# Kernel optimization log

Measured on AMD Instinct MI355X. Metric: run time of the kernel, lower is better.

Reference implementation:

```python
import jax, jax.numpy as jnp
import numpy as np

EPS = 1e-5


def _conv1x1(x, w, b):
    # x: (B,C,H,W), w: (O,C), b: (O,)
    return jnp.einsum('bchw,oc->bohw', x, w) + b[None, :, None, None]


def setup_inputs() -> dict:
    key = jax.random.key(0)
    ks = jax.random.split(key, 12)
    C, Ci = 512, 256
    B, H, W = 4, 64, 64
    s_in = 1.0 / np.sqrt(C)
    s_ci = 1.0 / np.sqrt(Ci)
    return {
        'x': jax.random.normal(ks[0], (B, C, H, W), dtype=jnp.float32),
        'g_w': jax.random.normal(ks[1], (Ci, C), dtype=jnp.float32) * s_in,
        'g_b': jax.random.normal(ks[2], (Ci,), dtype=jnp.float32) * 0.01,
        'theta_w': jax.random.normal(ks[3], (Ci, C), dtype=jnp.float32) * s_in,
        'theta_b': jax.random.normal(ks[4], (Ci,), dtype=jnp.float32) * 0.01,
        'phi_w': jax.random.normal(ks[5], (Ci, C), dtype=jnp.float32) * s_in,
        'phi_b': jax.random.normal(ks[6], (Ci,), dtype=jnp.float32) * 0.01,
        'W_w': jax.random.normal(ks[7], (C, Ci), dtype=jnp.float32) * s_ci,
        'W_b': jax.random.normal(ks[8], (C,), dtype=jnp.float32) * 0.01,
        'bn_gamma': jax.random.normal(ks[9], (C,), dtype=jnp.float32) * 0.1,
        'bn_beta': jax.random.normal(ks[10], (C,), dtype=jnp.float32) * 0.01,
    }


def reference(x, g_w, g_b, theta_w, theta_b, phi_w, phi_b, W_w, W_b, bn_gamma, bn_beta):
    B, C, H, W = x.shape
    Ci = g_w.shape[0]
    HW = H * W
    # 1x1-conv projections -> token form
    g = _conv1x1(x, g_w, g_b).reshape(B, Ci, HW).transpose(0, 2, 1)        # (B,HW,Ci)
    theta = _conv1x1(x, theta_w, theta_b).reshape(B, Ci, HW).transpose(0, 2, 1)  # (B,HW,Ci)
    phi = _conv1x1(x, phi_w, phi_b).reshape(B, Ci, HW)                      # (B,Ci,HW)
    # dense HWxHW attention, scaled by sqrt(inter_channels)
    pairwise = jnp.einsum('bnc,bcm->bnm', theta, phi) / jnp.sqrt(jnp.float32(Ci))
    attn = jax.nn.softmax(pairwise, axis=-1)
    y = jnp.einsum('bnm,bmc->bnc', attn, g)                                 # (B,HW,Ci)
    y = y.transpose(0, 2, 1).reshape(B, Ci, H, W)
    # output 1x1 conv + BatchNorm2d (training-mode batch statistics)
    z = _conv1x1(y, W_w, W_b)
    mean = jnp.mean(z, axis=(0, 2, 3), keepdims=True)
    var = jnp.var(z, axis=(0, 2, 3), keepdims=True)
    z = bn_gamma[None, :, None, None] * (z - mean) * jax.lax.rsqrt(var + EPS) + bn_beta[None, :, None, None]
    return z + x
```

## Files before the change

kernel.cpp:

```cpp
#include <hip/hip_runtime.h>

typedef unsigned short u16;
typedef __attribute__((ext_vector_type(4))) u16 u16x4;
typedef __attribute__((ext_vector_type(8))) u16 u16x8;
typedef __attribute__((ext_vector_type(8))) short s16x8;
typedef __attribute__((ext_vector_type(4))) float f32x4;

#define B_  4
#define C_  512
#define CI_ 256
#define HW_ 4096

static __device__ __forceinline__ u16 f2bf(float f) {
  unsigned u = __float_as_uint(f);
  return (u16)((u + 0x7FFFu + ((u >> 16) & 1u)) >> 16);
}
static __device__ __forceinline__ float bf2f(u16 h) {
  return __uint_as_float(((unsigned)h) << 16);
}

static __device__ __forceinline__ f32x4 mfma16(s16x8 a, s16x8 b, f32x4 c) {
  return __builtin_amdgcn_mfma_f32_16x16x32_bf16(a, b, c, 0, 0, 0);
}

typedef __attribute__((address_space(3))) unsigned int as3_u32;
typedef const __attribute__((address_space(1))) unsigned int as1_u32;
static __device__ __forceinline__ void gload16(const u16* g, u16* l) {
  __builtin_amdgcn_global_load_lds((as1_u32*)g, (as3_u32*)l, 16, 0, 0);
}

__global__ __launch_bounds__(256) void k0_wcvt(
    const float* __restrict__ wg, const float* __restrict__ wt,
    const float* __restrict__ wp, const float* __restrict__ Ww,
    u16* __restrict__ wB, u16* __restrict__ WwB)
{
  int idx = (blockIdx.x * 256 + threadIdx.x) * 8;
  const float* src;
  u16* dst;
  if (idx < 393216) {
    int r = idx >> 17;
    src = (r == 0 ? wg : r == 1 ? wt : wp) + (idx & 131071);
    dst = wB + idx;
  } else {
    src = Ww + (idx - 393216);
    dst = WwB + (idx - 393216);
  }
  float4 v0 = *reinterpret_cast<const float4*>(src);
  float4 v1 = *reinterpret_cast<const float4*>(src + 4);
  u16x8 h;
  h[0] = f2bf(v0.x); h[1] = f2bf(v0.y); h[2] = f2bf(v0.z); h[3] = f2bf(v0.w);
  h[4] = f2bf(v1.x); h[5] = f2bf(v1.y); h[6] = f2bf(v1.z); h[7] = f2bf(v1.w);
  *reinterpret_cast<u16x8*>(dst) = h;
}

__global__ __launch_bounds__(256) void k0_xt(
    const float* __restrict__ x, u16* __restrict__ xT, int b0)
{
  __shared__ u16 lds[64][72];
  const int tid = threadIdx.x;
  const int n0 = blockIdx.x * 64, c0 = blockIdx.y * 64;
  const int bl = blockIdx.z;
  const int b = b0 + bl;
  const int nc = (tid & 15) * 4;
#pragma unroll
  for (int i = 0; i < 4; ++i) {
    int cr = (tid >> 4) + i * 16;
    float4 v = *reinterpret_cast<const float4*>(
        &x[((size_t)(b * C_ + c0 + cr)) * HW_ + n0 + nc]);
    u16x4 h; h[0] = f2bf(v.x); h[1] = f2bf(v.y); h[2] = f2bf(v.z); h[3] = f2bf(v.w);
    *reinterpret_cast<u16x4*>(&lds[cr][nc]) = h;
  }
  __syncthreads();
  const int n = tid & 63, cg = tid >> 6;
  u16x8 o0, o1;
#pragma unroll
  for (int j = 0; j < 8; ++j) { o0[j] = lds[cg * 16 + j][n]; o1[j] = lds[cg * 16 + 8 + j][n]; }
  size_t dstb = ((size_t)bl * HW_ + n0 + n) * C_ + c0 + cg * 16;
  *reinterpret_cast<u16x8*>(&xT[dstb])     = o0;
  *reinterpret_cast<u16x8*>(&xT[dstb + 8]) = o1;
}

__global__ __launch_bounds__(256) void k1_proj(
    const u16* __restrict__ wB, const u16* __restrict__ xT,
    const float* __restrict__ bg, const float* __restrict__ bt, const float* __restrict__ bp,
    u16* __restrict__ g_s, u16* __restrict__ thetaT, u16* __restrict__ phiT, int half)
{
  extern __shared__ u16 sm1[];
  const int tid = threadIdx.x;
  const int lane = tid & 63, wid = tid >> 6;
  const int wm = wid >> 1, wn = wid & 1;
  const int l15 = lane & 15, g4 = lane >> 4;

  const int bid = blockIdx.x;
  const int r12 = bid % 12;
  const int nt = bid / 12;
  const int mt = r12 >> 1;
  const int bl = r12 & 1;
  const int b = half * 2 + bl;
  const int m0 = mt * 128, n0g = nt * 128;
  const int p = mt >> 1;

  const u16* xb = xT + (size_t)bl * HW_ * C_;

  const int srow = tid >> 2, sch = tid & 3;
  const u16* a_src = wB + (size_t)(m0 + srow) * C_ + sch * 8;
  const u16* b_src = xb + (size_t)(n0g + srow) * C_ + sch * 8;

  f32x4 acc[4][4] = {};

#pragma unroll
  for (int i = 0; i < 2; ++i) {
    gload16(a_src + (size_t)(i * 64) * C_, sm1 + (tid + i * 256) * 8);
    gload16(b_src + (size_t)(i * 64) * C_, sm1 + 4096 + (tid + i * 256) * 8);
  }
  __syncthreads();

  for (int ks = 0; ks < 16; ++ks) {
    const int cur = ks & 1;
    if (ks < 15) {
      const int nk = (ks + 1) * 32;
      u16* dA = sm1 + (cur ^ 1) * 8192;
#pragma unroll
      for (int i = 0; i < 2; ++i) {
        gload16(a_src + (size_t)(i * 64) * C_ + nk, dA + (tid + i * 256) * 8);
        gload16(b_src + (size_t)(i * 64) * C_ + nk, dA + 4096 + (tid + i * 256) * 8);
      }
    }
    const u16* A = sm1 + cur * 8192;
    const u16* Bt = A + 4096;
    s16x8 afr[4], bfr[4];
#pragma unroll
    for (int mf = 0; mf < 4; ++mf)
      afr[mf] = *reinterpret_cast<const s16x8*>(&A[(wm * 64 + mf * 16 + l15) * 32 + g4 * 8]);
#pragma unroll
    for (int nf = 0; nf < 4; ++nf)
      bfr[nf] = *reinterpret_cast<const s16x8*>(&Bt[(wn * 64 + nf * 16 + l15) * 32 + g4 * 8]);
#pragma unroll
    for (int mf = 0; mf < 4; ++mf)
#pragma unroll
      for (int nf = 0; nf < 4; ++nf)
        acc[mf][nf] = mfma16(afr[mf], bfr[nf], acc[mf][nf]);
    __syncthreads();
  }

  const float* bias = (p == 0) ? bg : (p == 1) ? bt : bp;
  const int cib = (mt & 1) * 128;
#pragma unroll
  for (int mf = 0; mf < 4; ++mf)
#pragma unroll
    for (int r = 0; r < 4; ++r) {
      float bv = bias[cib + wm * 64 + mf * 16 + g4 * 4 + r];
#pragma unroll
      for (int nf = 0; nf < 4; ++nf) acc[mf][nf][r] += bv;
    }

  if (p == 0) {
    u16* lds_t = sm1;
#pragma unroll
    for (int mf = 0; mf < 4; ++mf)
#pragma unroll
      for (int nf = 0; nf < 4; ++nf)
#pragma unroll
        for (int r = 0; r < 4; ++r)
          lds_t[(wm * 64 + mf * 16 + g4 * 4 + r) * 136 + wn * 64 + nf * 16 + l15] =
              f2bf(acc[mf][nf][r]);
    __syncthreads();
    const int m = tid >> 1, hh = tid & 1;
    size_t dst = ((size_t)b * CI_ + cib + m) * HW_ + n0g + hh * 64;
#pragma unroll
    for (int j = 0; j < 8; ++j)
      *reinterpret_cast<u16x8*>(&g_s[dst + j * 8]) =
          *reinterpret_cast<const u16x8*>(&lds_t[m * 136 + hh * 64 + j * 8]);
  } else {
    u16* outp = (p == 1) ? thetaT : phiT;
#pragma unroll
    for (int mf = 0; mf < 4; ++mf)
#pragma unroll
      for (int nf = 0; nf < 4; ++nf) {
        u16x4 h;
#pragma unroll
        for (int r = 0; r < 4; ++r) h[r] = f2bf(acc[mf][nf][r]);
        int n = n0g + wn * 64 + nf * 16 + l15;
        *reinterpret_cast<u16x4*>(
            &outp[((size_t)b * HW_ + n) * CI_ + cib + wm * 64 + mf * 16 + g4 * 4]) = h;
      }
  }
}

#define OFF_PHI0 0
#define OFF_PHI1 16384
#define OFF_G0   32768
#define OFF_G1   49152
#define OFF_PB0  65536
#define OFF_PB1  70144
#define OFF_LP   74752

__global__ __launch_bounds__(512) void k3_fused(
    const u16* __restrict__ thetaT, const u16* __restrict__ phiT,
    const u16* __restrict__ g_s, u16* __restrict__ y)
{
  extern __shared__ u16 smem[];
  float* Lp = (float*)(smem + OFF_LP);
  float* iL = Lp + 256;

  const int tid = threadIdx.x;
  const int lane = tid & 63, w = tid >> 6;
  const int l15 = lane & 15, g4 = lane >> 4;

  const int bid = blockIdx.x;
  const int xcd = bid & 7, slot = bid >> 3;
  const int b  = xcd >> 1;
  const int n0 = ((xcd & 1) * 32 + slot) * 64;

  const int ms = w >> 1, nh = w & 1;
  const int cq = w >> 1, nh2 = w & 1;

  const u16* thb = thetaT + (size_t)b * HW_ * CI_;
  const u16* phb = phiT   + (size_t)b * HW_ * CI_;
  const u16* gsb = g_s    + (size_t)b * CI_ * HW_;

  s16x8 thfr[2][8];
#pragma unroll
  for (int nf = 0; nf < 2; ++nf)
#pragma unroll
    for (int cs = 0; cs < 8; ++cs)
      thfr[nf][cs] = *reinterpret_cast<const s16x8*>(
          &thb[(size_t)(n0 + nh * 32 + nf * 16 + l15) * CI_ + cs * 32 + g4 * 8]);

  const int prow = tid >> 5, pj = tid & 31;
  const int grow = tid >> 3, gj = tid & 7;
  const u16* ph_src = phb + (size_t)prow * CI_ + ((pj ^ (prow & 7)) * 8);
  const u16* g_src  = gsb + (size_t)grow * HW_ + ((gj ^ (grow & 7)) * 8);
  const int ph_do = prow * 256 + pj * 8;
  const int g_do  = grow * 64  + gj * 8;

  auto stage_phi = [&](int off, int mt) {
#pragma unroll
    for (int i = 0; i < 4; ++i)
      gload16(ph_src + (size_t)(mt + i * 16) * CI_, smem + off + ph_do + i * 4096);
  };
  auto stage_g = [&](int off, int mt) {
#pragma unroll
    for (int i = 0; i < 4; ++i)
      gload16(g_src + mt + (size_t)i * 64 * HW_, smem + off + g_do + i * 4096);
  };

  f32x4 oacc[2][4] = {};
  float psum[2] = {0.f, 0.f};

  auto qk_phase = [&](const u16* phN, u16* pbN) {
    f32x4 acc[2] = {};
    __builtin_amdgcn_s_setprio(1);
#pragma unroll
    for (int cs = 0; cs < 8; ++cs) {
      s16x8 a = *reinterpret_cast<const s16x8*>(
          &phN[(ms * 16 + l15) * 256 + (((cs * 4 + g4) ^ (l15 & 7)) * 8)]);
      acc[0] = mfma16(a, thfr[0][cs], acc[0]);
      acc[1] = mfma16(a, thfr[1][cs], acc[1]);
    }
    __builtin_amdgcn_s_setprio(0);
#pragma unroll
    for (int nf = 0; nf < 2; ++nf) {
      u16x4 pk;
#pragma unroll
      for (int r = 0; r < 4; ++r) {
        float e = __expf(acc[nf][r] * 0.0625f);
        psum[nf] += e;
        pk[r] = f2bf(e);
      }
      *reinterpret_cast<u16x4*>(&pbN[(nh * 32 + nf * 16 + l15) * 72 + ms * 16 + g4 * 4]) = pk;
    }
  };
  auto pv_phase = [&](const u16* pbC, const u16* gC) {
    __builtin_amdgcn_s_setprio(1);
#pragma unroll
    for (int mk = 0; mk < 2; ++mk) {
      s16x8 pa[2];
#pragma unroll
      for (int nf = 0; nf < 2; ++nf)
        pa[nf] = *reinterpret_cast<const s16x8*>(
            &pbC[(nh2 * 32 + nf * 16 + l15) * 72 + mk * 32 + g4 * 8]);
#pragma unroll
      for (int cf = 0; cf < 4; ++cf) {
        int crow = cq * 64 + cf * 16 + l15;
        s16x8 bb = *reinterpret_cast<const s16x8*>(
            &gC[crow * 64 + (((mk * 4 + g4) ^ (crow & 7)) * 8)]);
        oacc[0][cf] = mfma16(pa[0], bb, oacc[0][cf]);
        oacc[1][cf] = mfma16(pa[1], bb, oacc[1][cf]);
      }
    }
    __builtin_amdgcn_s_setprio(0);
  };

  stage_phi(OFF_PHI0, 0); stage_g(OFF_G0, 0);
  stage_phi(OFF_PHI1, 64); stage_g(OFF_G1, 64);
  asm volatile("s_waitcnt vmcnt(0)" ::: "memory");
  __builtin_amdgcn_s_barrier();
  qk_phase(smem + OFF_PHI0, smem + OFF_PB0);
  asm volatile("s_waitcnt vmcnt(0) lgkmcnt(0)" ::: "memory");
  __builtin_amdgcn_s_barrier();

#pragma unroll 1
  for (int it = 0; it < 63; ++it) {
    const int cur = it & 1;
    if (it < 62) stage_phi(cur ? OFF_PHI1 : OFF_PHI0, (it + 2) * 64);
    qk_phase(smem + (cur ? OFF_PHI0 : OFF_PHI1),
             smem + (cur ? OFF_PB0 : OFF_PB1));
    pv_phase(smem + (cur ? OFF_PB1 : OFF_PB0),
             smem + (cur ? OFF_G1 : OFF_G0));
    asm volatile("s_waitcnt vmcnt(0) lgkmcnt(0)" ::: "memory");
    __builtin_amdgcn_s_barrier();
    if (it < 62) stage_g(cur ? OFF_G1 : OFF_G0, (it + 2) * 64);
  }
  pv_phase(smem + OFF_PB1, smem + OFF_G1);

#pragma unroll
  for (int nf = 0; nf < 2; ++nf) {
    psum[nf] += __shfl_xor(psum[nf], 16);
    psum[nf] += __shfl_xor(psum[nf], 32);
  }
  if (lane < 16) {
    Lp[ms * 64 + nh * 32 + lane]      = psum[0];
    Lp[ms * 64 + nh * 32 + 16 + lane] = psum[1];
  }
  __syncthreads();
  if (tid < 64) iL[tid] = 1.0f / (Lp[tid] + Lp[64 + tid] + Lp[128 + tid] + Lp[192 + tid]);
  __syncthreads();

  u16* yb = y + ((size_t)b * HW_ + n0) * CI_;
#pragma unroll
  for (int nf = 0; nf < 2; ++nf)
#pragma unroll
    for (int r = 0; r < 4; ++r) {
      int nl = nh2 * 32 + nf * 16 + g4 * 4 + r;
      float il = iL[nl];
#pragma unroll
      for (int cf = 0; cf < 4; ++cf)
        yb[(size_t)nl * CI_ + cq * 64 + cf * 16 + l15] = f2bf(oacc[nf][cf][r] * il);
    }
}

__global__ __launch_bounds__(256) void k4_wconv(
    const u16* __restrict__ WwB, const u16* __restrict__ y, const float* __restrict__ Wb,
    u16* __restrict__ z, float* __restrict__ zsum, float* __restrict__ zsq)
{
  extern __shared__ u16 sm4[];
  __shared__ float lds_ps[2][128][2];
  const int tid = threadIdx.x;
  const int lane = tid & 63, wid = tid >> 6;
  const int wm = wid >> 1, wn = wid & 1;
  const int l15 = lane & 15, g4 = lane >> 4;

  const int bid = blockIdx.x;
  const int xcd = bid & 7, slot = bid >> 3;
  const int b = xcd >> 1, half = xcd & 1;
  const int mt = slot & 3;
  const int nt = half * 16 + (slot >> 2);
  const int o0 = mt * 128, n0g = nt * 128;

  const int srow = tid >> 2, sch = tid & 3;
  const u16* a_src = WwB + (size_t)(o0 + srow) * CI_ + sch * 8;
  const u16* b_src = y + ((size_t)(b * HW_ + n0g + srow)) * CI_ + sch * 8;

  f32x4 acc[4][4] = {};

#pragma unroll
  for (int i = 0; i < 2; ++i) {
    gload16(a_src + (size_t)(i * 64) * CI_, sm4 + (tid + i * 256) * 8);
    gload16(b_src + (size_t)(i * 64) * CI_, sm4 + 4096 + (tid + i * 256) * 8);
  }
  __syncthreads();

  for (int ks = 0; ks < 8; ++ks) {
    const int cur = ks & 1;
    if (ks < 7) {
      const int nk = (ks + 1) * 32;
      u16* dA = sm4 + (cur ^ 1) * 8192;
#pragma unroll
      for (int i = 0; i < 2; ++i) {
        gload16(a_src + (size_t)(i * 64) * CI_ + nk, dA + (tid + i * 256) * 8);
        gload16(b_src + (size_t)(i * 64) * CI_ + nk, dA + 4096 + (tid + i * 256) * 8);
      }
    }
    const u16* A = sm4 + cur * 8192;
    const u16* Bt = A + 4096;
    s16x8 afr[4], bfr[4];
#pragma unroll
    for (int mf = 0; mf < 4; ++mf)
      afr[mf] = *reinterpret_cast<const s16x8*>(&A[(wm * 64 + mf * 16 + l15) * 32 + g4 * 8]);
#pragma unroll
    for (int nf = 0; nf < 4; ++nf)
      bfr[nf] = *reinterpret_cast<const s16x8*>(&Bt[(wn * 64 + nf * 16 + l15) * 32 + g4 * 8]);
#pragma unroll
    for (int mf = 0; mf < 4; ++mf)
#pragma unroll
      for (int nf = 0; nf < 4; ++nf)
        acc[mf][nf] = mfma16(afr[mf], bfr[nf], acc[mf][nf]);
    __syncthreads();
  }

  u16* lds_t = sm4;
#pragma unroll
  for (int mf = 0; mf < 4; ++mf)
#pragma unroll
    for (int r = 0; r < 4; ++r) {
      const int ol = wm * 64 + mf * 16 + g4 * 4 + r;
      float wb = Wb[o0 + ol];
      float s = 0.f, q = 0.f;
#pragma unroll
      for (int nf = 0; nf < 4; ++nf) {
        float zv = acc[mf][nf][r] + wb;
        s += zv; q += zv * zv;
        lds_t[ol * 136 + wn * 64 + nf * 16 + l15] = f2bf(zv);
      }
      s += __shfl_xor(s, 1); s += __shfl_xor(s, 2); s += __shfl_xor(s, 4); s += __shfl_xor(s, 8);
      q += __shfl_xor(q, 1); q += __shfl_xor(q, 2); q += __shfl_xor(q, 4); q += __shfl_xor(q, 8);
      if (l15 == 0) { lds_ps[wn][ol][0] = s; lds_ps[wn][ol][1] = q; }
    }
  __syncthreads();
  {
    const int m = tid >> 1, hh = tid & 1;
    size_t dst = ((size_t)(b * C_ + o0 + m)) * HW_ + n0g + hh * 64;
#pragma unroll
    for (int j = 0; j < 8; ++j)
      *reinterpret_cast<u16x8*>(&z[dst + j * 8]) =
          *reinterpret_cast<const u16x8*>(&lds_t[m * 136 + hh * 64 + j * 8]);
  }
  if (tid < 128) {
    int col = b * 32 + nt;
    zsum[(size_t)(o0 + tid) * 128 + col] = lds_ps[0][tid][0] + lds_ps[1][tid][0];
    zsq [(size_t)(o0 + tid) * 128 + col] = lds_ps[0][tid][1] + lds_ps[1][tid][1];
  }
}

__global__ void k5_bnstat(const float* __restrict__ zsum, const float* __restrict__ zsq,
                          const float* __restrict__ gamma, const float* __restrict__ beta,
                          float* __restrict__ bns, float* __restrict__ bnb)
{
  int ch = blockIdx.x * 256 + threadIdx.x;
  if (ch >= C_) return;
  float s = 0.f, q = 0.f;
  for (int i = 0; i < 128; ++i) { s += zsum[(size_t)ch * 128 + i]; q += zsq[(size_t)ch * 128 + i]; }
  const float inv_n = 1.0f / (B_ * HW_);
  float mean = s * inv_n;
  float var  = q * inv_n - mean * mean;
  float sc = gamma[ch] * rsqrtf(var + 1e-5f);
  bns[ch] = sc;
  bnb[ch] = beta[ch] - mean * sc;
}

__global__ __launch_bounds__(256) void k6_final(
    const u16* __restrict__ z, const float* __restrict__ x,
    const float* __restrict__ bns, const float* __restrict__ bnb,
    float* __restrict__ out)
{
  size_t i = ((size_t)blockIdx.x * 256 + threadIdx.x) * 8;
  int ch = (int)((i >> 12) & 511);
  float sc = bns[ch], sh = bnb[ch];
  u16x8 zv = *reinterpret_cast<const u16x8*>(&z[i]);
  float4 x0 = *reinterpret_cast<const float4*>(&x[i]);
  float4 x1 = *reinterpret_cast<const float4*>(&x[i + 4]);
  float4 o0, o1;
  o0.x = bf2f(zv[0]) * sc + sh + x0.x;
  o0.y = bf2f(zv[1]) * sc + sh + x0.y;
  o0.z = bf2f(zv[2]) * sc + sh + x0.z;
  o0.w = bf2f(zv[3]) * sc + sh + x0.w;
  o1.x = bf2f(zv[4]) * sc + sh + x1.x;
  o1.y = bf2f(zv[5]) * sc + sh + x1.y;
  o1.z = bf2f(zv[6]) * sc + sh + x1.z;
  o1.w = bf2f(zv[7]) * sc + sh + x1.w;
  *reinterpret_cast<float4*>(&out[i])     = o0;
  *reinterpret_cast<float4*>(&out[i + 4]) = o1;
}

extern "C" void kernel_launch(void* const* d_in, const int* in_sizes, int n_in,
                              void* d_out, int out_size, void* d_ws, size_t ws_size,
                              hipStream_t stream)
{
  (void)in_sizes; (void)n_in; (void)out_size; (void)ws_size;
  const float* x    = (const float*)d_in[0];
  const float* g_w  = (const float*)d_in[1];
  const float* g_b  = (const float*)d_in[2];
  const float* t_w  = (const float*)d_in[3];
  const float* t_b  = (const float*)d_in[4];
  const float* p_w  = (const float*)d_in[5];
  const float* p_b  = (const float*)d_in[6];
  const float* W_w  = (const float*)d_in[7];
  const float* W_b  = (const float*)d_in[8];
  const float* bng  = (const float*)d_in[9];
  const float* bnb_ = (const float*)d_in[10];

  char* ws = (char*)d_ws;
  const size_t M8 = (size_t)8 << 20;
  u16*   xT     = (u16*)(ws + 0);
  u16*   y      = (u16*)(ws + 0);
  u16*   thetaT = (u16*)(ws + M8);
  u16*   phiT   = (u16*)(ws + 2 * M8);
  u16*   g_s    = (u16*)(ws + 3 * M8);
  u16*   zbf    = (u16*)(ws + M8);
  float* zsum   = (float*)(ws + 3 * M8);
  float* zsq    = (float*)(ws + 3 * M8 + 262144);
  float* bnsV   = (float*)(ws + 3 * M8 + 524288);
  float* bnbV   = (float*)(ws + 3 * M8 + 526336);
  u16*   wB     = (u16*)(ws + 4 * M8);
  u16*   WwB    = (u16*)(ws + 4 * M8 + 786432);
  float* out    = (float*)d_out;

  const int k1_lds = 34816;
  const int k3_lds = 150784;
  const int k4_lds = 34816;
  hipFuncSetAttribute(reinterpret_cast<const void*>(k1_proj),
                      hipFuncAttributeMaxDynamicSharedMemorySize, k1_lds);
  hipFuncSetAttribute(reinterpret_cast<const void*>(k3_fused),
                      hipFuncAttributeMaxDynamicSharedMemorySize, k3_lds);
  hipFuncSetAttribute(reinterpret_cast<const void*>(k4_wconv),
                      hipFuncAttributeMaxDynamicSharedMemorySize, k4_lds);

  hipLaunchKernelGGL(k0_wcvt, dim3(256), dim3(256), 0, stream,
                     g_w, t_w, p_w, W_w, wB, WwB);
  for (int half = 0; half < 2; ++half) {
    hipLaunchKernelGGL(k0_xt, dim3(64, 8, 2), dim3(256), 0, stream, x, xT, half * 2);
    hipLaunchKernelGGL(k1_proj, dim3(384), dim3(256), k1_lds, stream,
                       wB, xT, g_b, t_b, p_b, g_s, thetaT, phiT, half);
  }
  hipLaunchKernelGGL(k3_fused, dim3(256), dim3(512), k3_lds, stream,
                     thetaT, phiT, g_s, y);
  hipLaunchKernelGGL(k4_wconv, dim3(512), dim3(256), k4_lds, stream,
                     WwB, y, W_b, zbf, zsum, zsq);
  hipLaunchKernelGGL(k5_bnstat, dim3(2), dim3(256), 0, stream,
                     zsum, zsq, bng, bnb_, bnsV, bnbV);
  hipLaunchKernelGGL(k6_final, dim3(4096), dim3(256), 0, stream,
                     zbf, x, bnsV, bnbV, out);
}
```

Before: 189.5 us.

## Triple-buffer GEMM prefetch and use partial vmcnt waits in attention loop

The projection and output-conv GEMMs move from a double-buffered loop with a full __syncthreads per step to a three-slot LDS ring. Each step waits with s_waitcnt vmcnt(4), so one stage of global loads stays in flight while the current tile is computed. The fused attention loop also stops draining all outstanding loads at every barrier: it waits only for the stage it needs and peels the final iterations. LDS per block grows for k1 and k4, which may lower occupancy, and the hand-counted vmcnt values must exactly match the number of loads issued per stage.

```diff
diff --git a/kernel.cpp b/kernel.cpp
--- a/kernel.cpp
+++ b/kernel.cpp
@@ -108,25 +108,16 @@
 
   f32x4 acc[4][4] = {};
 
-#pragma unroll
-  for (int i = 0; i < 2; ++i) {
-    gload16(a_src + (size_t)(i * 64) * C_, sm1 + (tid + i * 256) * 8);
-    gload16(b_src + (size_t)(i * 64) * C_, sm1 + 4096 + (tid + i * 256) * 8);
-  }
-  __syncthreads();
-
-  for (int ks = 0; ks < 16; ++ks) {
-    const int cur = ks & 1;
-    if (ks < 15) {
-      const int nk = (ks + 1) * 32;
-      u16* dA = sm1 + (cur ^ 1) * 8192;
-#pragma unroll
-      for (int i = 0; i < 2; ++i) {
-        gload16(a_src + (size_t)(i * 64) * C_ + nk, dA + (tid + i * 256) * 8);
-        gload16(b_src + (size_t)(i * 64) * C_ + nk, dA + 4096 + (tid + i * 256) * 8);
-      }
-    }
-    const u16* A = sm1 + cur * 8192;
+  auto stage1 = [&](int buf, int ks) {
+    u16* d = sm1 + buf * 8192;
+#pragma unroll
+    for (int i = 0; i < 2; ++i) {
+      gload16(a_src + (size_t)(i * 64) * C_ + ks * 32, d + (tid + i * 256) * 8);
+      gload16(b_src + (size_t)(i * 64) * C_ + ks * 32, d + 4096 + (tid + i * 256) * 8);
+    }
+  };
+  auto compute1 = [&](int buf) {
+    const u16* A = sm1 + buf * 8192;
     const u16* Bt = A + 4096;
     s16x8 afr[4], bfr[4];
 #pragma unroll
@@ -140,8 +131,22 @@
 #pragma unroll
       for (int nf = 0; nf < 4; ++nf)
         acc[mf][nf] = mfma16(afr[mf], bfr[nf], acc[mf][nf]);
-    __syncthreads();
-  }
+  };
+
+  stage1(0, 0); stage1(1, 1);
+  int cur = 0;
+#pragma unroll 1
+  for (int ks = 0; ks < 15; ++ks) {
+    asm volatile("s_waitcnt vmcnt(4)" ::: "memory");
+    __builtin_amdgcn_s_barrier();
+    compute1(cur);
+    if (ks < 14) { int nb = cur + 2; if (nb >= 3) nb -= 3; stage1(nb, ks + 2); }
+    cur = (cur == 2) ? 0 : cur + 1;
+  }
+  asm volatile("s_waitcnt vmcnt(0)" ::: "memory");
+  __builtin_amdgcn_s_barrier();
+  compute1(cur);
+  __syncthreads();
 
   const float* bias = (p == 0) ? bg : (p == 1) ? bt : bp;
   const int cib = (mt & 1) * 128;
@@ -297,21 +302,31 @@
   asm volatile("s_waitcnt vmcnt(0)" ::: "memory");
   __builtin_amdgcn_s_barrier();
   qk_phase(smem + OFF_PHI0, smem + OFF_PB0);
-  asm volatile("s_waitcnt vmcnt(0) lgkmcnt(0)" ::: "memory");
+  asm volatile("s_waitcnt lgkmcnt(0)" ::: "memory");
   __builtin_amdgcn_s_barrier();
 
 #pragma unroll 1
-  for (int it = 0; it < 63; ++it) {
+  for (int it = 0; it < 62; ++it) {
     const int cur = it & 1;
-    if (it < 62) stage_phi(cur ? OFF_PHI1 : OFF_PHI0, (it + 2) * 64);
+    stage_phi(cur ? OFF_PHI1 : OFF_PHI0, (it + 2) * 64);
+    asm volatile("s_waitcnt vmcnt(8)" ::: "memory");
+    __builtin_amdgcn_s_barrier();
     qk_phase(smem + (cur ? OFF_PHI0 : OFF_PHI1),
              smem + (cur ? OFF_PB0 : OFF_PB1));
     pv_phase(smem + (cur ? OFF_PB1 : OFF_PB0),
              smem + (cur ? OFF_G1 : OFF_G0));
-    asm volatile("s_waitcnt vmcnt(0) lgkmcnt(0)" ::: "memory");
+    asm volatile("s_waitcnt lgkmcnt(0)" ::: "memory");
     __builtin_amdgcn_s_barrier();
-    if (it < 62) stage_g(cur ? OFF_G1 : OFF_G0, (it + 2) * 64);
-  }
+    stage_g(cur ? OFF_G1 : OFF_G0, (it + 2) * 64);
+  }
+  asm volatile("s_waitcnt vmcnt(4)" ::: "memory");
+  __builtin_amdgcn_s_barrier();
+  qk_phase(smem + OFF_PHI1, smem + OFF_PB1);
+  pv_phase(smem + OFF_PB0, smem + OFF_G0);
+  asm volatile("s_waitcnt lgkmcnt(0)" ::: "memory");
+  __builtin_amdgcn_s_barrier();
+  asm volatile("s_waitcnt vmcnt(0)" ::: "memory");
+  __builtin_amdgcn_s_barrier();
   pv_phase(smem + OFF_PB1, smem + OFF_G1);
 
 #pragma unroll
@@ -364,25 +379,16 @@
 
   f32x4 acc[4][4] = {};
 
-#pragma unroll
-  for (int i = 0; i < 2; ++i) {
-    gload16(a_src + (size_t)(i * 64) * CI_, sm4 + (tid + i * 256) * 8);
-    gload16(b_src + (size_t)(i * 64) * CI_, sm4 + 4096 + (tid + i * 256) * 8);
-  }
-  __syncthreads();
-
-  for (int ks = 0; ks < 8; ++ks) {
-    const int cur = ks & 1;
-    if (ks < 7) {
-      const int nk = (ks + 1) * 32;
-      u16* dA = sm4 + (cur ^ 1) * 8192;
-#pragma unroll
-      for (int i = 0; i < 2; ++i) {
-        gload16(a_src + (size_t)(i * 64) * CI_ + nk, dA + (tid + i * 256) * 8);
-        gload16(b_src + (size_t)(i * 64) * CI_ + nk, dA + 4096 + (tid + i * 256) * 8);
-      }
-    }
-    const u16* A = sm4 + cur * 8192;
+  auto stage4 = [&](int buf, int ks) {
+    u16* d = sm4 + buf * 8192;
+#pragma unroll
+    for (int i = 0; i < 2; ++i) {
+      gload16(a_src + (size_t)(i * 64) * CI_ + ks * 32, d + (tid + i * 256) * 8);
+      gload16(b_src + (size_t)(i * 64) * CI_ + ks * 32, d + 4096 + (tid + i * 256) * 8);
+    }
+  };
+  auto compute4 = [&](int buf) {
+    const u16* A = sm4 + buf * 8192;
     const u16* Bt = A + 4096;
     s16x8 afr[4], bfr[4];
 #pragma unroll
@@ -396,8 +402,22 @@
 #pragma unroll
       for (int nf = 0; nf < 4; ++nf)
         acc[mf][nf] = mfma16(afr[mf], bfr[nf], acc[mf][nf]);
-    __syncthreads();
-  }
+  };
+
+  stage4(0, 0); stage4(1, 1);
+  int cur = 0;
+#pragma unroll 1
+  for (int ks = 0; ks < 7; ++ks) {
+    asm volatile("s_waitcnt vmcnt(4)" ::: "memory");
+    __builtin_amdgcn_s_barrier();
+    compute4(cur);
+    if (ks < 6) { int nb = cur + 2; if (nb >= 3) nb -= 3; stage4(nb, ks + 2); }
+    cur = (cur == 2) ? 0 : cur + 1;
+  }
+  asm volatile("s_waitcnt vmcnt(0)" ::: "memory");
+  __builtin_amdgcn_s_barrier();
+  compute4(cur);
+  __syncthreads();
 
   u16* lds_t = sm4;
 #pragma unroll
@@ -506,9 +526,9 @@
   u16*   WwB    = (u16*)(ws + 4 * M8 + 786432);
   float* out    = (float*)d_out;
 
-  const int k1_lds = 34816;
+  const int k1_lds = 49152;
   const int k3_lds = 150784;
-  const int k4_lds = 34816;
+  const int k4_lds = 49152;
   hipFuncSetAttribute(reinterpret_cast<const void*>(k1_proj),
                       hipFuncAttributeMaxDynamicSharedMemorySize, k1_lds);
   hipFuncSetAttribute(reinterpret_cast<const void*>(k3_fused),
```

New measurement: 198.0 us. +4.5%, slower.
